# Performance work log

Hardware: AMD Instinct MI355X
Metric: run time of the kernel (lower is better)

Reference implementation:

```python
import jax, jax.numpy as jnp
import numpy as np

H = 32        # num query heads
HKV = 8       # num kv heads
D = 128       # head_dim
SCALE = D ** -0.5
FP8_MAX = 448.0   # e4m3 max
EPS = 1e-8
PAGE = 256
NPAGES = 20
SQ = 1024     # new diffusion tokens
CTX = 3072    # cached context tokens
DIFF_BLK = 32 # diffusion block size


def setup_inputs() -> dict:
    key = jax.random.key(0)
    ks = jax.random.split(key, 6)
    q = jax.random.normal(ks[0], (SQ, H * D), dtype=jnp.float32)
    k = jax.random.normal(ks[1], (SQ, HKV * D), dtype=jnp.float32)
    v = jax.random.normal(ks[2], (SQ, HKV * D), dtype=jnp.float32)
    # paged caches (values already stored in quantized units)
    k_cache = jax.random.normal(ks[3], (NPAGES, PAGE, HKV, D), dtype=jnp.float32)
    v_cache = jax.random.normal(ks[4], (NPAGES, PAGE, HKV, D), dtype=jnp.float32)
    # new tokens go into slots right after the context
    slot_mapping = jnp.arange(CTX, CTX + SQ, dtype=jnp.int32)
    cache_slots = jnp.arange(CTX, dtype=jnp.int32)
    # diffusion mask: full visibility of context, block-causal among new tokens
    blk = jnp.arange(SQ) // DIFF_BLK
    ctx_mask = jnp.ones((SQ, CTX), dtype=bool)
    new_mask = blk[:, None] >= blk[None, :]
    block_mask = jnp.concatenate([ctx_mask, new_mask], axis=1)  # [SQ, CTX+SQ]
    return {"q": q, "k": k, "v": v, "k_cache": k_cache, "v_cache": v_cache,
            "slot_mapping": slot_mapping, "cache_slots": cache_slots,
            "block_mask": block_mask}


def reference(q, k, v, k_cache, v_cache, slot_mapping, cache_slots, block_mask):
    k3 = k.reshape(-1, HKV, D)
    v3 = v.reshape(-1, HKV, D)
    qh = q.reshape(-1, H, D)

    # ---- FP8 scale tracking: per-kv-head absmax over (token, dim) ----
    k_scale = jnp.maximum(jnp.max(jnp.abs(k3), axis=(0, 2)) / FP8_MAX, EPS)  # [HKV]
    v_scale = jnp.maximum(jnp.max(jnp.abs(v3), axis=(0, 2)) / FP8_MAX, EPS)

    # ---- paged KV-cache store with inline quantization ----
    kc = k_cache.reshape(-1, HKV, D)  # [NPAGES*PAGE, HKV, D]
    vc = v_cache.reshape(-1, HKV, D)
    k_q = jnp.clip(k3 / k_scale[None, :, None], -FP8_MAX, FP8_MAX)
    v_q = jnp.clip(v3 / v_scale[None, :, None], -FP8_MAX, FP8_MAX)
    kc = kc.at[slot_mapping].set(k_q)
    vc = vc.at[slot_mapping].set(v_q)

    # ---- load context tokens from cache and dequantize ----
    k_ctx = kc[cache_slots] * k_scale[None, :, None]  # [CTX, HKV, D]
    v_ctx = vc[cache_slots] * v_scale[None, :, None]
    k_comb = jnp.concatenate([k_ctx, k3], axis=0)  # [SKV, HKV, D]
    v_comb = jnp.concatenate([v_ctx, v3], axis=0)

    # ---- GQA flex attention with token-level block mask ----
    G = H // HKV
    k_g = jnp.repeat(k_comb, G, axis=1)  # [SKV, H, D]
    v_g = jnp.repeat(v_comb, G, axis=1)
    scores = jnp.einsum('qhd,khd->hqk', qh, k_g) * SCALE  # [H, SQ, SKV]
    scores = jnp.where(block_mask[None, :, :], scores, jnp.float32(-1e30))
    probs = jax.nn.softmax(scores, axis=-1)
    o = jnp.einsum('hqk,khd->qhd', probs, v_g)  # [SQ, H, D]
    return o.reshape(-1, H * D)
```

## Files before the change

kernel.cpp:

```cpp
#include <hip/hip_runtime.h>
#include <stdint.h>

#define H 32
#define HKV 8
#define D 128
#define SQ 1024
#define CTX 3072
#define SKV 4096
#define FP8_MAX_C 448.0f
#define EPS_C 1e-8f

typedef __attribute__((ext_vector_type(4))) float f32x4;
typedef __attribute__((ext_vector_type(8))) __bf16 bf16x8;
typedef __attribute__((ext_vector_type(8))) unsigned short u16x8;
typedef __attribute__((ext_vector_type(4))) unsigned short u16x4;

__device__ __forceinline__ unsigned short f2bf(float x) {
  unsigned int u = __builtin_bit_cast(unsigned int, x);
  u += 0x7fffu + ((u >> 16) & 1u);
  return (unsigned short)(u >> 16);
}

__device__ __forceinline__ f32x4 mfma16(bf16x8 a, bf16x8 b, f32x4 c) {
  return __builtin_amdgcn_mfma_f32_16x16x32_bf16(a, b, c, 0, 0, 0);
}

__device__ __forceinline__ void gld16(const unsigned short* g, char* l) {
  __builtin_amdgcn_global_load_lds(
      (const __attribute__((address_space(1))) unsigned int*)g,
      (__attribute__((address_space(3))) unsigned int*)l, 16, 0, 0);
}

__device__ __forceinline__ void stage_sync() {
  asm volatile("s_waitcnt vmcnt(0)" ::: "memory");
  __builtin_amdgcn_sched_barrier(0);
  __syncthreads();
}

__global__ void scales_part(const float* __restrict__ k,
                            const float* __restrict__ v,
                            unsigned int* __restrict__ smax) {
  const int b = blockIdx.x & 15;
  const int part = blockIdx.x >> 4;
  const float* src = (b < HKV) ? k : v;
  const int h = b & 7;
  const int tid = threadIdx.x;
  const int d0 = (tid & 31) * 4;
  float mx = 0.f;
  const int t1 = part * 128 + 128;
  for (int t = part * 128 + (tid >> 5); t < t1; t += 8) {
    float4 vv = *reinterpret_cast<const float4*>(src + (size_t)t * (HKV * D) + h * D + d0);
    mx = fmaxf(mx, fmaxf(fmaxf(fabsf(vv.x), fabsf(vv.y)),
                         fmaxf(fabsf(vv.z), fabsf(vv.w))));
  }
  __shared__ float red[256];
  red[tid] = mx;
  __syncthreads();
  for (int s = 128; s > 0; s >>= 1) {
    if (tid < s) red[tid] = fmaxf(red[tid], red[tid + s]);
    __syncthreads();
  }
  if (tid == 0) atomicMax(&smax[b], __float_as_uint(red[0]));
}

__global__ void scales_fin(const unsigned int* __restrict__ smax,
                           float* __restrict__ scales) {
  const int i = threadIdx.x;
  if (i < 16) scales[i] = fmaxf(__uint_as_float(smax[i]) / FP8_MAX_C, EPS_C);
}

__global__ void prep_k(const float* __restrict__ k,
                       const float* __restrict__ k_cache,
                       const int* __restrict__ cache_slots,
                       const float* __restrict__ scales,
                       unsigned short* __restrict__ k_comb) {
  const int tid = blockIdx.x * 256 + threadIdx.x;
  const int d8 = tid & 15;
  const int t = (tid >> 4) & (SKV - 1);
  const int h = tid >> 16;
  const int d0 = d8 * 8;
  const float* src;
  float mul;
  if (t < CTX) {
    int slot = cache_slots[t];
    src = k_cache + (size_t)slot * (HKV * D) + h * D + d0;
    mul = scales[h];
  } else {
    src = k + (size_t)(t - CTX) * (HKV * D) + h * D + d0;
    mul = 1.f;
  }
  float4 a = *reinterpret_cast<const float4*>(src);
  float4 bb = *reinterpret_cast<const float4*>(src + 4);
  u16x8 r;
  r[0] = f2bf(a.x * mul);  r[1] = f2bf(a.y * mul);
  r[2] = f2bf(a.z * mul);  r[3] = f2bf(a.w * mul);
  r[4] = f2bf(bb.x * mul); r[5] = f2bf(bb.y * mul);
  r[6] = f2bf(bb.z * mul); r[7] = f2bf(bb.w * mul);
  *reinterpret_cast<u16x8*>(k_comb + ((size_t)h * SKV + t) * D + d0) = r;
}

__global__ void prep_v(const float* __restrict__ v,
                       const float* __restrict__ v_cache,
                       const int* __restrict__ cache_slots,
                       const float* __restrict__ scales,
                       unsigned short* __restrict__ v_combT) {
  const int tid = blockIdx.x * 256 + threadIdx.x;
  const int d = tid & 127;
  const int t8 = (tid >> 7) & 511;
  const int h = tid >> 16;
  const int t0 = t8 * 8;
  const float sc = scales[8 + h];
  u16x8 r;
#pragma unroll
  for (int i = 0; i < 8; ++i) {
    int t = t0 + i;
    float val;
    if (t < CTX) {
      int slot = cache_slots[t];
      val = v_cache[(size_t)slot * (HKV * D) + h * D + d] * sc;
    } else {
      val = v[(size_t)(t - CTX) * (HKV * D) + h * D + d];
    }
    r[i] = f2bf(val);
  }
  *reinterpret_cast<u16x8*>(v_combT + ((size_t)h * D + d) * SKV + t0) = r;
}

#define LDBF(p) (*reinterpret_cast<const bf16x8*>(p))
#define Z4 ((f32x4){0.f, 0.f, 0.f, 0.f})

#define STAGE(TB, BUFO)                                                        \
  {                                                                            \
    _Pragma("unroll")                                                          \
    for (int j = 0; j < 4; ++j) {                                              \
      const int c = wid * 256 + j * 64 + l;                                    \
      const int r_ = c >> 4;                                                   \
      const int lc_ = (c & 15) ^ (r_ & 7);                                     \
      gld16(kb + (size_t)((TB) + r_) * D + lc_ * 8,                            \
            smem + (BUFO) + c * 16);                                           \
      const int dv_ = c >> 3;                                                  \
      const int lv_ = (c & 7) ^ (dv_ & 7);                                     \
      gld16(vb + (size_t)dv_ * SKV + (TB) + lv_ * 8,                           \
            smem + (BUFO) + 16384 + c * 16);                                   \
    }                                                                          \
  }

#define PK(SREG, PKREG, RSV)                                                   \
  {                                                                            \
    float p0_ = __builtin_amdgcn_exp2f(SREG[0] - m);                           \
    float p1_ = __builtin_amdgcn_exp2f(SREG[1] - m);                           \
    float p2_ = __builtin_amdgcn_exp2f(SREG[2] - m);                           \
    float p3_ = __builtin_amdgcn_exp2f(SREG[3] - m);                           \
    RSV += (p0_ + p1_) + (p2_ + p3_);                                          \
    PKREG[0] = f2bf(p0_); PKREG[1] = f2bf(p1_);                                \
    PKREG[2] = f2bf(p2_); PKREG[3] = f2bf(p3_);                                \
  }

#define QKSF(SF, SA, SB)                                                       \
  {                                                                            \
    bf16x8 a0 = LDBF(kc + SF * 4096 + kx0);                                    \
    bf16x8 a1 = LDBF(kc + SF * 4096 + kx1);                                    \
    bf16x8 a2 = LDBF(kc + SF * 4096 + kx2);                                    \
    bf16x8 a3 = LDBF(kc + SF * 4096 + kx3);                                    \
    SA = mfma16(a0, qa0, SA); SA = mfma16(a1, qa1, SA);                        \
    SA = mfma16(a2, qa2, SA); SA = mfma16(a3, qa3, SA);                        \
    SB = mfma16(a0, qb0, SB); SB = mfma16(a1, qb1, SB);                        \
    SB = mfma16(a2, qb2, SB); SB = mfma16(a3, qb3, SB);                        \
  }

#define PVDT(DT, AA, AB)                                                       \
  {                                                                            \
    bf16x8 va = LDBF(vc + DT * 2048 + vxa);                                    \
    bf16x8 vw = LDBF(vc + DT * 2048 + vxb);                                    \
    AA = mfma16(pfa0, va, AA); AA = mfma16(pfa1, vw, AA);                      \
    AB = mfma16(pfb0, va, AB); AB = mfma16(pfb1, vw, AB);                      \
  }

__launch_bounds__(256, 2)
__global__ void attn_kernel(const float* __restrict__ q,
                            const unsigned short* __restrict__ k_comb,
                            const unsigned short* __restrict__ v_combT,
                            float* __restrict__ out,
                            float* __restrict__ part1,
                            float* __restrict__ ml) {
  extern __shared__ __align__(16) char smem[];
  const int bid = blockIdx.x;
  const int hkv = bid & 7;
  const int qp = (bid >> 3) & 31;
  const int half = bid >> 8;
  const int tid = threadIdx.x;
  const int wid = tid >> 6;
  const int l = tid & 63;
  const int lo = l & 15;
  const int g = l >> 4;
  const int qbase = qp * 32 + (wid >> 1) * 16;
  const int hqa = hkv * 4 + (wid & 1) * 2;
  const int nt32 = 97 + qp;
  const int n64 = (nt32 + 1) >> 1;
  const int nh = (n64 + 1) >> 1;
  const int t0 = half ? nh : 0;
  const int t1 = half ? n64 : nh;
  const bool tail = (nt32 & 1) && half;

  const unsigned short* kb = k_comb + (size_t)hkv * SKV * D;
  const unsigned short* vb = v_combT + (size_t)hkv * D * SKV;

  bf16x8 qa0, qa1, qa2, qa3, qb0, qb1, qb2, qb3;
  {
    const float qs = 0.088388347648318447f * 1.4426950408889634f;
    const float* qpA = q + (size_t)(qbase + lo) * (H * D) + hqa * D;
#define QLOAD(PTR, KS, DST)                                                    \
    {                                                                          \
      float4 a = *reinterpret_cast<const float4*>((PTR) + KS * 32 + g * 8);    \
      float4 b = *reinterpret_cast<const float4*>((PTR) + KS * 32 + g * 8 + 4);\
      union { unsigned short u[8]; bf16x8 v; } f;                              \
      f.u[0] = f2bf(a.x * qs); f.u[1] = f2bf(a.y * qs);                        \
      f.u[2] = f2bf(a.z * qs); f.u[3] = f2bf(a.w * qs);                        \
      f.u[4] = f2bf(b.x * qs); f.u[5] = f2bf(b.y * qs);                        \
      f.u[6] = f2bf(b.z * qs); f.u[7] = f2bf(b.w * qs);                        \
      DST = f.v;                                                               \
    }
    QLOAD(qpA, 0, qa0) QLOAD(qpA, 1, qa1) QLOAD(qpA, 2, qa2) QLOAD(qpA, 3, qa3)
    const float* qpB = qpA + D;
    QLOAD(qpB, 0, qb0) QLOAD(qpB, 1, qb1) QLOAD(qpB, 2, qb2) QLOAD(qpB, 3, qb3)
#undef QLOAD
  }

  f32x4 aa0 = Z4, aa1 = Z4, aa2 = Z4, aa3 = Z4;
  f32x4 aa4 = Z4, aa5 = Z4, aa6 = Z4, aa7 = Z4;
  f32x4 ab0 = Z4, ab1 = Z4, ab2 = Z4, ab3 = Z4;
  f32x4 ab4 = Z4, ab5 = Z4, ab6 = Z4, ab7 = Z4;
  float m = -1e30f;
  float lsa = 0.f, lsb = 0.f;

  const int xr = lo & 7;
  const int kx0 = ((0 + g) ^ xr) << 4;
  const int kx1 = ((4 + g) ^ xr) << 4;
  const int kx2 = ((8 + g) ^ xr) << 4;
  const int kx3 = ((12 + g) ^ xr) << 4;
  const int vxa = ((g) ^ xr) << 4;
  const int vxb = ((g + 4) ^ xr) << 4;
  const char* kbl = smem + lo * 256;
  const char* vbl = smem + 16384 + lo * 128;
  const int xsw = (lo & 7) << 4;
  char* pbA = smem + 65536 + (wid * 2 + 0) * 2048 + lo * 128;
  char* pbB = smem + 65536 + (wid * 2 + 1) * 2048 + lo * 128;

  int cur = 0;
  STAGE(t0 * 64, 0)
  stage_sync();

  for (int t = t0; t < t1; ++t) {
    if (t + 1 < t1) STAGE((t + 1) * 64, (cur ^ 1) * 32768)

    const char* kc = kbl + cur * 32768;
    const char* vc = vbl + cur * 32768;

    f32x4 sa0 = Z4, sa1 = Z4, sa2 = Z4, sa3 = Z4;
    f32x4 sb0 = Z4, sb1 = Z4, sb2 = Z4, sb3 = Z4;
    QKSF(0, sa0, sb0)
    QKSF(1, sa1, sb1)
    QKSF(2, sa2, sb2)
    QKSF(3, sa3, sb3)

    if (tail && t == n64 - 1) {
      sa2 = (f32x4){-1e30f, -1e30f, -1e30f, -1e30f};
      sa3 = (f32x4){-1e30f, -1e30f, -1e30f, -1e30f};
      sb2 = (f32x4){-1e30f, -1e30f, -1e30f, -1e30f};
      sb3 = (f32x4){-1e30f, -1e30f, -1e30f, -1e30f};
    }

    float pmax = fmaxf(fmaxf(fmaxf(sa0[0], sa0[1]), fmaxf(sa0[2], sa0[3])),
                       fmaxf(fmaxf(sa1[0], sa1[1]), fmaxf(sa1[2], sa1[3])));
    pmax = fmaxf(pmax,
                 fmaxf(fmaxf(fmaxf(sa2[0], sa2[1]), fmaxf(sa2[2], sa2[3])),
                       fmaxf(fmaxf(sa3[0], sa3[1]), fmaxf(sa3[2], sa3[3]))));
    pmax = fmaxf(pmax,
                 fmaxf(fmaxf(fmaxf(sb0[0], sb0[1]), fmaxf(sb0[2], sb0[3])),
                       fmaxf(fmaxf(sb1[0], sb1[1]), fmaxf(sb1[2], sb1[3]))));
    pmax = fmaxf(pmax,
                 fmaxf(fmaxf(fmaxf(sb2[0], sb2[1]), fmaxf(sb2[2], sb2[3])),
                       fmaxf(fmaxf(sb3[0], sb3[1]), fmaxf(sb3[2], sb3[3]))));
    if (!__all(pmax - m <= 8.f)) {
      float rm = fmaxf(pmax, __shfl_xor(pmax, 16));
      rm = fmaxf(rm, __shfl_xor(rm, 32));
      float mn = fmaxf(m, rm);
      float scl = __builtin_amdgcn_exp2f(m - mn);
      lsa *= scl; lsb *= scl;
      aa0 *= scl; aa1 *= scl; aa2 *= scl; aa3 *= scl;
      aa4 *= scl; aa5 *= scl; aa6 *= scl; aa7 *= scl;
      ab0 *= scl; ab1 *= scl; ab2 *= scl; ab3 *= scl;
      ab4 *= scl; ab5 *= scl; ab6 *= scl; ab7 *= scl;
      m = mn;
    }

    u16x4 ka0, ka1, ka2, ka3, kb0, kb1, kb2, kb3;
    PK(sa0, ka0, lsa) PK(sa1, ka1, lsa) PK(sa2, ka2, lsa) PK(sa3, ka3, lsa)
    PK(sb0, kb0, lsb) PK(sb1, kb1, lsb) PK(sb2, kb2, lsb) PK(sb3, kb3, lsb)

    *reinterpret_cast<u16x4*>(pbA + ((0 * 32 + g * 8) ^ xsw)) = ka0;
    *reinterpret_cast<u16x4*>(pbA + ((1 * 32 + g * 8) ^ xsw)) = ka1;
    *reinterpret_cast<u16x4*>(pbA + ((2 * 32 + g * 8) ^ xsw)) = ka2;
    *reinterpret_cast<u16x4*>(pbA + ((3 * 32 + g * 8) ^ xsw)) = ka3;
    *reinterpret_cast<u16x4*>(pbB + ((0 * 32 + g * 8) ^ xsw)) = kb0;
    *reinterpret_cast<u16x4*>(pbB + ((1 * 32 + g * 8) ^ xsw)) = kb1;
    *reinterpret_cast<u16x4*>(pbB + ((2 * 32 + g * 8) ^ xsw)) = kb2;
    *reinterpret_cast<u16x4*>(pbB + ((3 * 32 + g * 8) ^ xsw)) = kb3;
    bf16x8 pfa0 = LDBF(pbA + ((g * 16) ^ xsw));
    bf16x8 pfa1 = LDBF(pbA + ((64 + g * 16) ^ xsw));
    bf16x8 pfb0 = LDBF(pbB + ((g * 16) ^ xsw));
    bf16x8 pfb1 = LDBF(pbB + ((64 + g * 16) ^ xsw));

    PVDT(0, aa0, ab0)
    PVDT(1, aa1, ab1)
    PVDT(2, aa2, ab2)
    PVDT(3, aa3, ab3)
    PVDT(4, aa4, ab4)
    PVDT(5, aa5, ab5)
    PVDT(6, aa6, ab6)
    PVDT(7, aa7, ab7)

    stage_sync();
    cur ^= 1;
  }

  lsa += __shfl_xor(lsa, 16); lsa += __shfl_xor(lsa, 32);
  lsb += __shfl_xor(lsb, 16); lsb += __shfl_xor(lsb, 32);
  float* dst = half ? part1 : out;
  if (g == 0) {
    float2 v;
    v.x = m; v.y = lsa;
    *reinterpret_cast<float2*>(ml + ((size_t)half * SQ * H + (qbase + lo) * H + hqa) * 2) = v;
    v.y = lsb;
    *reinterpret_cast<float2*>(ml + ((size_t)half * SQ * H + (qbase + lo) * H + hqa + 1) * 2) = v;
  }
#pragma unroll
  for (int r = 0; r < 4; ++r) {
    float* opa = dst + (size_t)(qbase + g * 4 + r) * (H * D) + hqa * D + lo;
    float* opb = opa + D;
    opa[0 * 16] = aa0[r]; opb[0 * 16] = ab0[r];
    opa[1 * 16] = aa1[r]; opb[1 * 16] = ab1[r];
    opa[2 * 16] = aa2[r]; opb[2 * 16] = ab2[r];
    opa[3 * 16] = aa3[r]; opb[3 * 16] = ab3[r];
    opa[4 * 16] = aa4[r]; opb[4 * 16] = ab4[r];
    opa[5 * 16] = aa5[r]; opb[5 * 16] = ab5[r];
    opa[6 * 16] = aa6[r]; opb[6 * 16] = ab6[r];
    opa[7 * 16] = aa7[r]; opb[7 * 16] = ab7[r];
  }
}

__global__ void merge_kernel(float* __restrict__ out,
                             const float* __restrict__ part1,
                             const float* __restrict__ ml) {
  const int idx = blockIdx.x * 256 + threadIdx.x;
  const int h = (idx >> 5) & 31;
  const int qrow = idx >> 10;
  const float2* mp = (const float2*)ml;
  float2 A = mp[qrow * H + h];
  float2 B = mp[SQ * H + qrow * H + h];
  float mm = fmaxf(A.x, B.x);
  float wa = __builtin_amdgcn_exp2f(A.x - mm);
  float wb = __builtin_amdgcn_exp2f(B.x - mm);
  float inv = 1.f / (A.y * wa + B.y * wb);
  float4 oa = reinterpret_cast<float4*>(out)[idx];
  float4 ob = reinterpret_cast<const float4*>(part1)[idx];
  float4 r;
  r.x = (oa.x * wa + ob.x * wb) * inv;
  r.y = (oa.y * wa + ob.y * wb) * inv;
  r.z = (oa.z * wa + ob.z * wb) * inv;
  r.w = (oa.w * wa + ob.w * wb) * inv;
  reinterpret_cast<float4*>(out)[idx] = r;
}

extern "C" void kernel_launch(void* const* d_in, const int* in_sizes, int n_in,
                              void* d_out, int out_size, void* d_ws, size_t ws_size,
                              hipStream_t stream) {
  (void)in_sizes; (void)n_in; (void)out_size; (void)ws_size;
  const float* q = (const float*)d_in[0];
  const float* k = (const float*)d_in[1];
  const float* v = (const float*)d_in[2];
  const float* k_cache = (const float*)d_in[3];
  const float* v_cache = (const float*)d_in[4];
  const int* cache_slots = (const int*)d_in[6];
  float* out = (float*)d_out;

  unsigned int* smax = (unsigned int*)d_ws;
  float* scales = (float*)((char*)d_ws + 64);
  unsigned short* k_comb = (unsigned short*)((char*)d_ws + 256);
  unsigned short* v_combT = k_comb + (size_t)HKV * SKV * D;
  float* part1 = (float*)((char*)d_ws + 256 + (size_t)32 * 1024 * 1024 / 2);
  float* ml = part1 + (size_t)SQ * H * D;

  hipMemsetAsync(smax, 0, 64, stream);
  scales_part<<<128, 256, 0, stream>>>(k, v, smax);
  scales_fin<<<1, 64, 0, stream>>>(smax, scales);
  prep_k<<<2048, 256, 0, stream>>>(k, k_cache, cache_slots, scales, k_comb);
  prep_v<<<2048, 256, 0, stream>>>(v, v_cache, cache_slots, scales, v_combT);
  attn_kernel<<<512, 256, 81920, stream>>>(q, k_comb, v_combT, out, part1, ml);
  merge_kernel<<<4096, 256, 0, stream>>>(out, part1, ml);
}
```

Baseline: 119.1 us.

## Transpose softmax probabilities in registers via permlane swaps instead of LDS

Replaces the LDS round-trip that converted the P fragment from the QK accumulator layout to the PV operand layout with packed bf16 conversions and v_permlane32/16 swaps in registers. This removes the per-tile LDS stores and loads, and shrinks dynamic shared memory from 80KB to 64KB, which may allow higher occupancy. It also raises wave priority around the MFMA blocks and reverses the q-block order for the second half of the KV split so the two halves pair differently across the grid. The risk is a lane-mapping error in the register transpose, and rounding may differ slightly from the old software bf16 conversion.

```diff
diff --git a/kernel.cpp b/kernel.cpp
--- a/kernel.cpp
+++ b/kernel.cpp
@@ -13,7 +13,6 @@
 typedef __attribute__((ext_vector_type(4))) float f32x4;
 typedef __attribute__((ext_vector_type(8))) __bf16 bf16x8;
 typedef __attribute__((ext_vector_type(8))) unsigned short u16x8;
-typedef __attribute__((ext_vector_type(4))) unsigned short u16x4;
 
 __device__ __forceinline__ unsigned short f2bf(float x) {
   unsigned int u = __builtin_bit_cast(unsigned int, x);
@@ -145,15 +144,37 @@
     }                                                                          \
   }
 
-#define PK(SREG, PKREG, RSV)                                                   \
+#define EXP4(SREG, P, RSV)                                                     \
   {                                                                            \
-    float p0_ = __builtin_amdgcn_exp2f(SREG[0] - m);                           \
-    float p1_ = __builtin_amdgcn_exp2f(SREG[1] - m);                           \
-    float p2_ = __builtin_amdgcn_exp2f(SREG[2] - m);                           \
-    float p3_ = __builtin_amdgcn_exp2f(SREG[3] - m);                           \
-    RSV += (p0_ + p1_) + (p2_ + p3_);                                          \
-    PKREG[0] = f2bf(p0_); PKREG[1] = f2bf(p1_);                                \
-    PKREG[2] = f2bf(p2_); PKREG[3] = f2bf(p3_);                                \
+    P[0] = __builtin_amdgcn_exp2f(SREG[0] - m);                                \
+    P[1] = __builtin_amdgcn_exp2f(SREG[1] - m);                                \
+    P[2] = __builtin_amdgcn_exp2f(SREG[2] - m);                                \
+    P[3] = __builtin_amdgcn_exp2f(SREG[3] - m);                                \
+    RSV += (P[0] + P[1]) + (P[2] + P[3]);                                      \
+  }
+
+#define CVTPK(DST, LO, HI)                                                     \
+  asm("v_cvt_pk_bf16_f32 %0, %1, %2" : "=v"(DST) : "v"(LO), "v"(HI));
+#define SW32(A, B)                                                             \
+  asm("v_permlane32_swap_b32 %0, %1" : "+v"(A), "+v"(B));
+#define SW16(A, B)                                                             \
+  asm("v_permlane16_swap_b32 %0, %1" : "+v"(A), "+v"(B));
+
+#define PTRANS(P0, P1, P2, P3, PF0, PF1)                                       \
+  {                                                                            \
+    unsigned int A_, Ap_, B_, Bp_, C_, Cp_, Dd_, Dp_;                          \
+    CVTPK(A_, P0[0], P0[1]) CVTPK(Ap_, P0[2], P0[3])                           \
+    CVTPK(B_, P1[0], P1[1]) CVTPK(Bp_, P1[2], P1[3])                           \
+    CVTPK(C_, P2[0], P2[1]) CVTPK(Cp_, P2[2], P2[3])                           \
+    CVTPK(Dd_, P3[0], P3[1]) CVTPK(Dp_, P3[2], P3[3])                          \
+    SW32(A_, B_) SW16(A_, B_)                                                  \
+    SW32(Ap_, Bp_) SW16(Ap_, Bp_)                                              \
+    SW32(C_, Dd_) SW16(C_, Dd_)                                                \
+    SW32(Cp_, Dp_) SW16(Cp_, Dp_)                                              \
+    union { unsigned int d[4]; bf16x8 v; } u0_, u1_;                           \
+    u0_.d[0] = A_; u0_.d[1] = Ap_; u0_.d[2] = B_; u0_.d[3] = Bp_;              \
+    u1_.d[0] = C_; u1_.d[1] = Cp_; u1_.d[2] = Dd_; u1_.d[3] = Dp_;             \
+    PF0 = u0_.v; PF1 = u1_.v;                                                  \
   }
 
 #define QKSF(SF, SA, SB)                                                       \
@@ -186,8 +207,9 @@
   extern __shared__ __align__(16) char smem[];
   const int bid = blockIdx.x;
   const int hkv = bid & 7;
-  const int qp = (bid >> 3) & 31;
+  const int qp_raw = (bid >> 3) & 31;
   const int half = bid >> 8;
+  const int qp = half ? (31 - qp_raw) : qp_raw;
   const int tid = threadIdx.x;
   const int wid = tid >> 6;
   const int l = tid & 63;
@@ -242,9 +264,6 @@
   const int vxb = ((g + 4) ^ xr) << 4;
   const char* kbl = smem + lo * 256;
   const char* vbl = smem + 16384 + lo * 128;
-  const int xsw = (lo & 7) << 4;
-  char* pbA = smem + 65536 + (wid * 2 + 0) * 2048 + lo * 128;
-  char* pbB = smem + 65536 + (wid * 2 + 1) * 2048 + lo * 128;
 
   int cur = 0;
   STAGE(t0 * 64, 0)
@@ -258,10 +277,12 @@
 
     f32x4 sa0 = Z4, sa1 = Z4, sa2 = Z4, sa3 = Z4;
     f32x4 sb0 = Z4, sb1 = Z4, sb2 = Z4, sb3 = Z4;
+    __builtin_amdgcn_s_setprio(1);
     QKSF(0, sa0, sb0)
     QKSF(1, sa1, sb1)
     QKSF(2, sa2, sb2)
     QKSF(3, sa3, sb3)
+    __builtin_amdgcn_s_setprio(0);
 
     if (tail && t == n64 - 1) {
       sa2 = (f32x4){-1e30f, -1e30f, -1e30f, -1e30f};
@@ -294,23 +315,15 @@
       m = mn;
     }
 
-    u16x4 ka0, ka1, ka2, ka3, kb0, kb1, kb2, kb3;
-    PK(sa0, ka0, lsa) PK(sa1, ka1, lsa) PK(sa2, ka2, lsa) PK(sa3, ka3, lsa)
-    PK(sb0, kb0, lsb) PK(sb1, kb1, lsb) PK(sb2, kb2, lsb) PK(sb3, kb3, lsb)
-
-    *reinterpret_cast<u16x4*>(pbA + ((0 * 32 + g * 8) ^ xsw)) = ka0;
-    *reinterpret_cast<u16x4*>(pbA + ((1 * 32 + g * 8) ^ xsw)) = ka1;
-    *reinterpret_cast<u16x4*>(pbA + ((2 * 32 + g * 8) ^ xsw)) = ka2;
-    *reinterpret_cast<u16x4*>(pbA + ((3 * 32 + g * 8) ^ xsw)) = ka3;
-    *reinterpret_cast<u16x4*>(pbB + ((0 * 32 + g * 8) ^ xsw)) = kb0;
-    *reinterpret_cast<u16x4*>(pbB + ((1 * 32 + g * 8) ^ xsw)) = kb1;
-    *reinterpret_cast<u16x4*>(pbB + ((2 * 32 + g * 8) ^ xsw)) = kb2;
-    *reinterpret_cast<u16x4*>(pbB + ((3 * 32 + g * 8) ^ xsw)) = kb3;
-    bf16x8 pfa0 = LDBF(pbA + ((g * 16) ^ xsw));
-    bf16x8 pfa1 = LDBF(pbA + ((64 + g * 16) ^ xsw));
-    bf16x8 pfb0 = LDBF(pbB + ((g * 16) ^ xsw));
-    bf16x8 pfb1 = LDBF(pbB + ((64 + g * 16) ^ xsw));
-
+    float pa0[4], pa1[4], pa2[4], pa3[4], pb0[4], pb1[4], pb2[4], pb3[4];
+    EXP4(sa0, pa0, lsa) EXP4(sa1, pa1, lsa) EXP4(sa2, pa2, lsa) EXP4(sa3, pa3, lsa)
+    EXP4(sb0, pb0, lsb) EXP4(sb1, pb1, lsb) EXP4(sb2, pb2, lsb) EXP4(sb3, pb3, lsb)
+
+    bf16x8 pfa0, pfa1, pfb0, pfb1;
+    PTRANS(pa0, pa1, pa2, pa3, pfa0, pfa1)
+    PTRANS(pb0, pb1, pb2, pb3, pfb0, pfb1)
+
+    __builtin_amdgcn_s_setprio(1);
     PVDT(0, aa0, ab0)
     PVDT(1, aa1, ab1)
     PVDT(2, aa2, ab2)
@@ -319,6 +332,7 @@
     PVDT(5, aa5, ab5)
     PVDT(6, aa6, ab6)
     PVDT(7, aa7, ab7)
+    __builtin_amdgcn_s_setprio(0);
 
     stage_sync();
     cur ^= 1;
@@ -396,6 +410,6 @@
   scales_fin<<<1, 64, 0, stream>>>(smax, scales);
   prep_k<<<2048, 256, 0, stream>>>(k, k_cache, cache_slots, scales, k_comb);
   prep_v<<<2048, 256, 0, stream>>>(v, v_cache, cache_slots, scales, v_combT);
-  attn_kernel<<<512, 256, 81920, stream>>>(q, k_comb, v_combT, out, part1, ml);
+  attn_kernel<<<512, 256, 65536, stream>>>(q, k_comb, v_combT, out, part1, ml);
   merge_kernel<<<4096, 256, 0, stream>>>(out, part1, ml);
 }
```

Measured after the change: 113.9 us. -4.4%, faster.
